# Optimization experiments

Measured on AMD Instinct MI355X. Metric: run time of the kernel, lower is better.

Reference implementation:

```python
import jax, jax.numpy as jnp
import numpy as np

CD_W1 = 1.0
CD_W2 = 1.0


def setup_inputs() -> dict:
    key = jax.random.key(0)
    k1, k2 = jax.random.split(key)
    B, N, M, D = 16, 4096, 4096, 3
    points1 = jax.random.normal(k1, (B, N, D), dtype=jnp.float32)
    points2 = jax.random.normal(k2, (B, M, D), dtype=jnp.float32)
    return {"points1": points1, "points2": points2}


def reference(points1, points2):
    # squared pairwise distances via |a|^2 + |b|^2 - 2 a.b (GEMM form)
    a2 = jnp.sum(points1 * points1, axis=-1)          # [B, N]
    b2 = jnp.sum(points2 * points2, axis=-1)          # [B, M]
    ab = jnp.einsum("bnd,bmd->bnm", points1, points2)  # [B, N, M]
    dist = a2[:, :, None] + b2[:, None, :] - 2.0 * ab   # [B, N, M]
    dist_min1 = jnp.min(dist, axis=2)                  # nearest in points2 for each point1
    dist_min2 = jnp.min(dist, axis=1)                  # nearest in points1 for each point2
    B = points1.shape[0]
    return (CD_W1 * jnp.sum(dist_min1) + CD_W2 * jnp.sum(dist_min2)) / B
```

## Files before the change

kernel.cpp:

```cpp
#include <hip/hip_runtime.h>

#define BQ     16
#define NPTS   4096
#define TOTAL  (BQ * NPTS)
#define NPART  128
#define SIDE_TILES    (TOTAL / 16)
#define PANEL_U4_SIDE ((size_t)SIDE_TILES * 32)
#define WS_MIN_BYTES  ((size_t)2 * TOTAL * 4)
#define WS_NEED (WS_MIN_BYTES + 2 * PANEL_U4_SIDE * 16 + (size_t)NPART * 4)

typedef __attribute__((ext_vector_type(8))) short short8;
typedef __attribute__((ext_vector_type(4))) float f32x4;

__device__ __forceinline__ unsigned short f2bf(float x) {
    union { float f; unsigned u; } v; v.f = x;
    unsigned r = v.u + 0x7FFFu + ((v.u >> 16) & 1u);
    return (unsigned short)(r >> 16);
}
__device__ __forceinline__ float bf2f(unsigned short h) {
    union { float f; unsigned u; } v; v.u = ((unsigned)h) << 16; return v.f;
}
#define BF_ONE 0x3F80

__device__ __forceinline__ uint4 make_bslots16(const float* __restrict__ pts,
                                               int tile, int lane32) {
    const int g = lane32 >> 4;
    const float* pp = pts + (size_t)(tile * 16 + (lane32 & 15)) * 3;
    const float x = pp[0], y = pp[1], z = pp[2];
    const unsigned short xh = f2bf(x), yh = f2bf(y), zh = f2bf(z);
    const unsigned short xl = f2bf(x - bf2f(xh)), yl = f2bf(y - bf2f(yh)),
                         zl = f2bf(z - bf2f(zh));
    const unsigned short m2xh = f2bf(-2.0f * bf2f(xh)), m2yh = f2bf(-2.0f * bf2f(yh)),
                         m2zh = f2bf(-2.0f * bf2f(zh));
    const unsigned short m2xl = f2bf(-2.0f * bf2f(xl)), m2yl = f2bf(-2.0f * bf2f(yl)),
                         m2zl = f2bf(-2.0f * bf2f(zl));
    const float s2 = fmaf(x, x, fmaf(y, y, z * z));
    const unsigned short s2h = f2bf(s2);
    const unsigned short s2l = f2bf(s2 - bf2f(s2h));
    unsigned short s[8];
    if (g == 0) { s[0]=m2xh; s[1]=m2yh; s[2]=m2zh; s[3]=m2xl;   s[4]=m2yl;   s[5]=m2zl; s[6]=m2xh; s[7]=m2yh; }
    else        { s[0]=m2zh; s[1]=BF_ONE; s[2]=BF_ONE; s[3]=s2h; s[4]=s2l;   s[5]=0;    s[6]=0;    s[7]=0;    }
    uint4 o;
    o.x = (unsigned)s[0] | ((unsigned)s[1] << 16);
    o.y = (unsigned)s[2] | ((unsigned)s[3] << 16);
    o.z = (unsigned)s[4] | ((unsigned)s[5] << 16);
    o.w = (unsigned)s[6] | ((unsigned)s[7] << 16);
    return o;
}

__device__ __forceinline__ short8 make_aslots16(const float* __restrict__ pts,
                                                int point, int g) {
    const float* pp = pts + (size_t)point * 3;
    const float x = pp[0], y = pp[1], z = pp[2];
    const unsigned short xh = f2bf(x), yh = f2bf(y), zh = f2bf(z);
    const unsigned short xl = f2bf(x - bf2f(xh)), yl = f2bf(y - bf2f(yh)),
                         zl = f2bf(z - bf2f(zh));
    const float s2 = fmaf(x, x, fmaf(y, y, z * z));
    const unsigned short s2h = f2bf(s2);
    const unsigned short s2l = f2bf(s2 - bf2f(s2h));
    unsigned short s[8];
    if (g == 0) { s[0]=xh; s[1]=yh; s[2]=zh; s[3]=xh;     s[4]=yh;     s[5]=zh; s[6]=xl; s[7]=yl; }
    else        { s[0]=zl; s[1]=s2h; s[2]=s2l; s[3]=BF_ONE; s[4]=BF_ONE; s[5]=0; s[6]=0; s[7]=0; }
    union { unsigned u[4]; short8 v; } o;
    o.u[0] = (unsigned)s[0] | ((unsigned)s[1] << 16);
    o.u[1] = (unsigned)s[2] | ((unsigned)s[3] << 16);
    o.u[2] = (unsigned)s[4] | ((unsigned)s[5] << 16);
    o.u[3] = (unsigned)s[6] | ((unsigned)s[7] << 16);
    return o.v;
}

__global__ __launch_bounds__(256) void cd_prep(const float* __restrict__ p1,
                                               const float* __restrict__ p2,
                                               unsigned* __restrict__ wsmin,
                                               uint4* __restrict__ panels) {
    const int tid = blockIdx.x * 256 + threadIdx.x;
    if (tid < 2 * TOTAL) wsmin[tid] = 0x7F800000u;
    const int side = tid >> 17;
    const int l    = tid & 131071;
    const float* pts = side ? p2 : p1;
    panels[tid] = make_bslots16(pts, l >> 5, l & 31);
}

__global__ __launch_bounds__(256, 4) void cd_pass(
        const float* __restrict__ p1, const float* __restrict__ p2,
        const uint4* __restrict__ panels, unsigned* __restrict__ wsmin) {
    const int dir  = blockIdx.y;
    const float* __restrict__ A = dir ? p2 : p1;
    const uint4* __restrict__ panel = panels + (dir ? 0 : PANEL_U4_SIDE);
    unsigned* __restrict__ outmin = wsmin + dir * TOTAL;

    const int bx   = blockIdx.x;
    const int b    = bx >> 5;
    const int rg   = (bx >> 2) & 7;
    const int cg   = bx & 3;
    const int wave = threadIdx.x >> 6;
    const int lane = threadIdx.x & 63;
    const int half = lane >> 5;

    const int rowbase = b * NPTS + rg * 512 + wave * 128;

    short8 az; { union { unsigned u[4]; short8 v; } z = {{0,0,0,0}}; az = z.v; }
    short8 a0=az,a1=az,a2=az,a3=az,a4=az,a5=az,a6=az,a7=az;
    if (half == 0) {
        const int g = (lane >> 4) & 1, r = lane & 15;
        a0 = make_aslots16(A, rowbase +   0 + r, g);
        a1 = make_aslots16(A, rowbase +  16 + r, g);
        a2 = make_aslots16(A, rowbase +  32 + r, g);
        a3 = make_aslots16(A, rowbase +  48 + r, g);
        a4 = make_aslots16(A, rowbase +  64 + r, g);
        a5 = make_aslots16(A, rowbase +  80 + r, g);
        a6 = make_aslots16(A, rowbase +  96 + r, g);
        a7 = make_aslots16(A, rowbase + 112 + r, g);
    }

    f32x4 zero = {0.0f, 0.0f, 0.0f, 0.0f};
    f32x4 r0,r1,r2,r3,r4,r5,r6,r7;
#pragma unroll
    for (int e = 0; e < 4; ++e) {
        r0[e]=3.0e38f; r1[e]=3.0e38f; r2[e]=3.0e38f; r3[e]=3.0e38f;
        r4[e]=3.0e38f; r5[e]=3.0e38f; r6[e]=3.0e38f; r7[e]=3.0e38f;
    }

    const uint4* __restrict__ bp =
        panel + (size_t)(b * 256 + cg * 64) * 32 + (lane & 31);

#define CD_COMPUTE(C0, C1)                                                   \
    do {                                                                     \
        const short8 bf0 = *reinterpret_cast<const short8*>(&(C0));          \
        const short8 bf1 = *reinterpret_cast<const short8*>(&(C1));          \
        f32x4 d0, d1;                                                        \
        d0 = __builtin_amdgcn_mfma_f32_16x16x32_bf16(a0, bf0, zero, 0,0,0);  \
        d1 = __builtin_amdgcn_mfma_f32_16x16x32_bf16(a0, bf1, zero, 0,0,0);  \
        _Pragma("unroll") for (int e = 0; e < 4; ++e)                        \
            r0[e] = fminf(r0[e], fminf(d0[e], d1[e]));                       \
        d0 = __builtin_amdgcn_mfma_f32_16x16x32_bf16(a1, bf0, zero, 0,0,0);  \
        d1 = __builtin_amdgcn_mfma_f32_16x16x32_bf16(a1, bf1, zero, 0,0,0);  \
        _Pragma("unroll") for (int e = 0; e < 4; ++e)                        \
            r1[e] = fminf(r1[e], fminf(d0[e], d1[e]));                       \
        d0 = __builtin_amdgcn_mfma_f32_16x16x32_bf16(a2, bf0, zero, 0,0,0);  \
        d1 = __builtin_amdgcn_mfma_f32_16x16x32_bf16(a2, bf1, zero, 0,0,0);  \
        _Pragma("unroll") for (int e = 0; e < 4; ++e)                        \
            r2[e] = fminf(r2[e], fminf(d0[e], d1[e]));                       \
        d0 = __builtin_amdgcn_mfma_f32_16x16x32_bf16(a3, bf0, zero, 0,0,0);  \
        d1 = __builtin_amdgcn_mfma_f32_16x16x32_bf16(a3, bf1, zero, 0,0,0);  \
        _Pragma("unroll") for (int e = 0; e < 4; ++e)                        \
            r3[e] = fminf(r3[e], fminf(d0[e], d1[e]));                       \
        d0 = __builtin_amdgcn_mfma_f32_16x16x32_bf16(a4, bf0, zero, 0,0,0);  \
        d1 = __builtin_amdgcn_mfma_f32_16x16x32_bf16(a4, bf1, zero, 0,0,0);  \
        _Pragma("unroll") for (int e = 0; e < 4; ++e)                        \
            r4[e] = fminf(r4[e], fminf(d0[e], d1[e]));                       \
        d0 = __builtin_amdgcn_mfma_f32_16x16x32_bf16(a5, bf0, zero, 0,0,0);  \
        d1 = __builtin_amdgcn_mfma_f32_16x16x32_bf16(a5, bf1, zero, 0,0,0);  \
        _Pragma("unroll") for (int e = 0; e < 4; ++e)                        \
            r5[e] = fminf(r5[e], fminf(d0[e], d1[e]));                       \
        d0 = __builtin_amdgcn_mfma_f32_16x16x32_bf16(a6, bf0, zero, 0,0,0);  \
        d1 = __builtin_amdgcn_mfma_f32_16x16x32_bf16(a6, bf1, zero, 0,0,0);  \
        _Pragma("unroll") for (int e = 0; e < 4; ++e)                        \
            r6[e] = fminf(r6[e], fminf(d0[e], d1[e]));                       \
        d0 = __builtin_amdgcn_mfma_f32_16x16x32_bf16(a7, bf0, zero, 0,0,0);  \
        d1 = __builtin_amdgcn_mfma_f32_16x16x32_bf16(a7, bf1, zero, 0,0,0);  \
        _Pragma("unroll") for (int e = 0; e < 4; ++e)                        \
            r7[e] = fminf(r7[e], fminf(d0[e], d1[e]));                       \
    } while (0)

    uint4 c0 = bp[0], c1 = bp[32];
    size_t off = 64;
#pragma unroll 1
    for (int i = 0; i < 31; ++i) {
        uint4 n0 = bp[off], n1 = bp[off + 32];
        off += 64;
        CD_COMPUTE(c0, c1);
        c0 = n0; c1 = n1;
    }
    CD_COMPUTE(c0, c1);
#undef CD_COMPUTE

    const int rgrp = lane >> 4;
#pragma unroll
    for (int s = 0; s < 8; ++s) {
        f32x4 rv = (s==0)?r0:(s==1)?r1:(s==2)?r2:(s==3)?r3:(s==4)?r4:(s==5)?r5:(s==6)?r6:r7;
#pragma unroll
        for (int e = 0; e < 4; ++e) {
            float v = rv[e];
            v = fminf(v, __shfl_xor(v, 1));
            v = fminf(v, __shfl_xor(v, 2));
            v = fminf(v, __shfl_xor(v, 4));
            v = fminf(v, __shfl_xor(v, 8));
            if ((lane & 15) == 0)
                atomicMin(&outmin[rowbase + s * 16 + rgrp * 4 + e],
                          __float_as_uint(fmaxf(v, 0.0f)));
        }
    }
}

__global__ __launch_bounds__(256) void cd_reduce1(const float* __restrict__ wsmin,
                                                  float* __restrict__ partial) {
    __shared__ float sred[256];
    const float4* __restrict__ v = (const float4*)wsmin;
    const int i = blockIdx.x * 256 + threadIdx.x;
    float4 x = v[i];
    sred[threadIdx.x] = (x.x + x.y) + (x.z + x.w);
    __syncthreads();
    for (int st = 128; st > 0; st >>= 1) {
        if (threadIdx.x < st) sred[threadIdx.x] += sred[threadIdx.x + st];
        __syncthreads();
    }
    if (threadIdx.x == 0) partial[blockIdx.x] = sred[0];
}

__global__ __launch_bounds__(NPART) void cd_reduce2(const float* __restrict__ partial,
                                                    float* __restrict__ out) {
    __shared__ float sred[NPART];
    sred[threadIdx.x] = partial[threadIdx.x];
    __syncthreads();
    for (int st = NPART / 2; st > 0; st >>= 1) {
        if (threadIdx.x < st) sred[threadIdx.x] += sred[threadIdx.x + st];
        __syncthreads();
    }
    if (threadIdx.x == 0) out[0] = sred[0] * (1.0f / (float)BQ);
}

__global__ __launch_bounds__(256) void cd_init_ws(unsigned int* __restrict__ ws) {
    ws[blockIdx.x * 256 + threadIdx.x] = 0x7F800000u;
}
#define F_APT 8
__global__ __launch_bounds__(256) void cd_min_lds(
        const float* __restrict__ p1, const float* __restrict__ p2,
        unsigned int* __restrict__ wsmin) {
    const int dir = blockIdx.y;
    const float* __restrict__ Aset = dir ? p2 : p1;
    const float* __restrict__ Bset = dir ? p1 : p2;
    unsigned int* __restrict__ outmin = wsmin + dir * TOTAL;
    const int atile = blockIdx.x / 16;
    const int mtile = blockIdx.x % 16;
    const int a0 = atile * 2048;
    const int m0 = (a0 / NPTS) * NPTS + mtile * 256;
    __shared__ float4 sbf[256];
    {
        const float* bpn = Bset + (size_t)(m0 + threadIdx.x) * 3;
        float bx = bpn[0], by = bpn[1], bz = bpn[2];
        sbf[threadIdx.x] = make_float4(-2.0f*bx, -2.0f*by, -2.0f*bz,
                                       fmaf(bx,bx,fmaf(by,by,bz*bz)));
    }
    __syncthreads();
    float ax[F_APT], ay[F_APT], az_[F_APT], q2[F_APT], mn[F_APT];
#pragma unroll
    for (int k = 0; k < F_APT; ++k) {
        const int ai = a0 + k*256 + threadIdx.x;
        const float* ap = Aset + (size_t)ai * 3;
        ax[k]=ap[0]; ay[k]=ap[1]; az_[k]=ap[2];
        q2[k]=fmaf(ax[k],ax[k],fmaf(ay[k],ay[k],az_[k]*az_[k]));
        mn[k]=3.0e38f;
    }
#pragma unroll 2
    for (int j = 0; j < 256; j += 2) {
        const float4 b0 = sbf[j], b1 = sbf[j+1];
#pragma unroll
        for (int k = 0; k < F_APT; ++k) {
            float d0 = fmaf(az_[k],b0.z,b0.w); d0=fmaf(ay[k],b0.y,d0); d0=fmaf(ax[k],b0.x,d0);
            float d1 = fmaf(az_[k],b1.z,b1.w); d1=fmaf(ay[k],b1.y,d1); d1=fmaf(ax[k],b1.x,d1);
            mn[k] = fminf(fminf(mn[k], d0), d1);
        }
    }
#pragma unroll
    for (int k = 0; k < F_APT; ++k) {
        const int ai = a0 + k*256 + threadIdx.x;
        atomicMin(&outmin[ai], __float_as_uint(fmaxf(q2[k]+mn[k], 0.0f)));
    }
}
__global__ __launch_bounds__(1024) void cd_reduce_single(const float* __restrict__ wsmin,
                                                         float* __restrict__ out) {
    __shared__ float sred[1024];
    const float4* __restrict__ v = (const float4*)wsmin;
    float s = 0.0f;
    for (int i = threadIdx.x; i < (2*TOTAL)/4; i += 1024) {
        float4 x = v[i]; s += (x.x + x.y) + (x.z + x.w);
    }
    sred[threadIdx.x] = s;
    __syncthreads();
    for (int st = 512; st > 0; st >>= 1) {
        if (threadIdx.x < st) sred[threadIdx.x] += sred[threadIdx.x + st];
        __syncthreads();
    }
    if (threadIdx.x == 0) out[0] = sred[0] * (1.0f / (float)BQ);
}

extern "C" void kernel_launch(void* const* d_in, const int* in_sizes, int n_in,
                              void* d_out, int out_size, void* d_ws, size_t ws_size,
                              hipStream_t stream) {
    const float* p1 = (const float*)d_in[0];
    const float* p2 = (const float*)d_in[1];
    float* out = (float*)d_out;

    if (ws_size >= WS_NEED) {
        unsigned* wsmin = (unsigned*)d_ws;
        uint4* panels  = (uint4*)((char*)d_ws + WS_MIN_BYTES);
        float* partial = (float*)((char*)d_ws + WS_MIN_BYTES + 2 * PANEL_U4_SIDE * 16);

        cd_prep<<<1024, 256, 0, stream>>>(p1, p2, wsmin, panels);
        dim3 grid(512, 2, 1);
        cd_pass<<<grid, 256, 0, stream>>>(p1, p2, panels, wsmin);
        cd_reduce1<<<128, 256, 0, stream>>>((const float*)wsmin, partial);
        cd_reduce2<<<1, NPART, 0, stream>>>(partial, out);
    } else {
        unsigned* wsmin = (unsigned*)d_ws;
        cd_init_ws<<<(2 * TOTAL) / 256, 256, 0, stream>>>(wsmin);
        dim3 grid(512, 2, 1);
        cd_min_lds<<<grid, 256, 0, stream>>>(p1, p2, wsmin);
        cd_reduce_single<<<1, 1024, 0, stream>>>((const float*)wsmin, out);
    }
}
```

Before: 43.39 us.

## Fuse panel prep into main kernel via LDS and replace atomics with partial-min buffers

After: 41.96 us. -3.3%, faster.

```diff
diff --git a/kernel.cpp b/kernel.cpp
--- a/kernel.cpp
+++ b/kernel.cpp
@@ -4,10 +4,9 @@
 #define NPTS   4096
 #define TOTAL  (BQ * NPTS)
 #define NPART  128
-#define SIDE_TILES    (TOTAL / 16)
-#define PANEL_U4_SIDE ((size_t)SIDE_TILES * 32)
-#define WS_MIN_BYTES  ((size_t)2 * TOTAL * 4)
-#define WS_NEED (WS_MIN_BYTES + 2 * PANEL_U4_SIDE * 16 + (size_t)NPART * 4)
+
+#define ROWMIN_FLOATS ((size_t)8 * TOTAL)
+#define WS_NEED (ROWMIN_FLOATS * 4 + (size_t)NPART * 4)
 
 typedef __attribute__((ext_vector_type(8))) short short8;
 typedef __attribute__((ext_vector_type(4))) float f32x4;
@@ -69,25 +68,12 @@
     return o.v;
 }
 
-__global__ __launch_bounds__(256) void cd_prep(const float* __restrict__ p1,
-                                               const float* __restrict__ p2,
-                                               unsigned* __restrict__ wsmin,
-                                               uint4* __restrict__ panels) {
-    const int tid = blockIdx.x * 256 + threadIdx.x;
-    if (tid < 2 * TOTAL) wsmin[tid] = 0x7F800000u;
-    const int side = tid >> 17;
-    const int l    = tid & 131071;
-    const float* pts = side ? p2 : p1;
-    panels[tid] = make_bslots16(pts, l >> 5, l & 31);
-}
-
-__global__ __launch_bounds__(256, 4) void cd_pass(
+__global__ __launch_bounds__(256, 4) void cd_main(
         const float* __restrict__ p1, const float* __restrict__ p2,
-        const uint4* __restrict__ panels, unsigned* __restrict__ wsmin) {
+        float* __restrict__ rowmin) {
     const int dir  = blockIdx.y;
-    const float* __restrict__ A = dir ? p2 : p1;
-    const uint4* __restrict__ panel = panels + (dir ? 0 : PANEL_U4_SIDE);
-    unsigned* __restrict__ outmin = wsmin + dir * TOTAL;
+    const float* __restrict__ A  = dir ? p2 : p1;
+    const float* __restrict__ Bp = dir ? p1 : p2;
 
     const int bx   = blockIdx.x;
     const int b    = bx >> 5;
@@ -96,6 +82,15 @@
     const int wave = threadIdx.x >> 6;
     const int lane = threadIdx.x & 63;
     const int half = lane >> 5;
+
+    __shared__ uint4 spanel[64 * 32];
+
+    const float* __restrict__ Bbase = Bp + (size_t)(b * NPTS + cg * 1024) * 3;
+#pragma unroll
+    for (int k = 0; k < 8; ++k) {
+        const int s = threadIdx.x + k * 256;
+        spanel[s] = make_bslots16(Bbase, s >> 5, s & 31);
+    }
 
     const int rowbase = b * NPTS + rg * 512 + wave * 128;
 
@@ -121,8 +116,7 @@
         r4[e]=3.0e38f; r5[e]=3.0e38f; r6[e]=3.0e38f; r7[e]=3.0e38f;
     }
 
-    const uint4* __restrict__ bp =
-        panel + (size_t)(b * 256 + cg * 64) * 32 + (lane & 31);
+    __syncthreads();
 
 #define CD_COMPUTE(C0, C1)                                                   \
     do {                                                                     \
@@ -163,18 +157,21 @@
             r7[e] = fminf(r7[e], fminf(d0[e], d1[e]));                       \
     } while (0)
 
-    uint4 c0 = bp[0], c1 = bp[32];
-    size_t off = 64;
+    const int sl = lane & 31;
+    int idx = wave * 16;
+    uint4 c0 = spanel[idx * 32 + sl], c1 = spanel[(idx + 1) * 32 + sl];
 #pragma unroll 1
     for (int i = 0; i < 31; ++i) {
-        uint4 n0 = bp[off], n1 = bp[off + 32];
-        off += 64;
+        const int nidx = (idx + 2) & 63;
+        uint4 n0 = spanel[nidx * 32 + sl];
+        uint4 n1 = spanel[(nidx + 1) * 32 + sl];
         CD_COMPUTE(c0, c1);
-        c0 = n0; c1 = n1;
+        c0 = n0; c1 = n1; idx = nidx;
     }
     CD_COMPUTE(c0, c1);
 #undef CD_COMPUTE
 
+    float* __restrict__ outr = rowmin + (size_t)(dir * 4 + cg) * TOTAL;
     const int rgrp = lane >> 4;
 #pragma unroll
     for (int s = 0; s < 8; ++s) {
@@ -187,19 +184,26 @@
             v = fminf(v, __shfl_xor(v, 4));
             v = fminf(v, __shfl_xor(v, 8));
             if ((lane & 15) == 0)
-                atomicMin(&outmin[rowbase + s * 16 + rgrp * 4 + e],
-                          __float_as_uint(fmaxf(v, 0.0f)));
+                outr[rowbase + s * 16 + rgrp * 4 + e] = fmaxf(v, 0.0f);
         }
     }
 }
 
-__global__ __launch_bounds__(256) void cd_reduce1(const float* __restrict__ wsmin,
+__global__ __launch_bounds__(256) void cd_combine(const float* __restrict__ rowmin,
                                                   float* __restrict__ partial) {
     __shared__ float sred[256];
-    const float4* __restrict__ v = (const float4*)wsmin;
-    const int i = blockIdx.x * 256 + threadIdx.x;
-    float4 x = v[i];
-    sred[threadIdx.x] = (x.x + x.y) + (x.z + x.w);
+    const int tid = blockIdx.x * 256 + threadIdx.x;
+    float s = 0.0f;
+#pragma unroll
+    for (int k = 0; k < 4; ++k) {
+        const int i   = tid + k * 32768;
+        const int d   = i >> 16;
+        const int row = i & (TOTAL - 1);
+        const float* base = rowmin + (size_t)d * 4 * TOTAL + row;
+        s += fminf(fminf(base[0], base[TOTAL]),
+                   fminf(base[2 * TOTAL], base[3 * TOTAL]));
+    }
+    sred[threadIdx.x] = s;
     __syncthreads();
     for (int st = 128; st > 0; st >>= 1) {
         if (threadIdx.x < st) sred[threadIdx.x] += sred[threadIdx.x + st];
@@ -208,8 +212,8 @@
     if (threadIdx.x == 0) partial[blockIdx.x] = sred[0];
 }
 
-__global__ __launch_bounds__(NPART) void cd_reduce2(const float* __restrict__ partial,
-                                                    float* __restrict__ out) {
+__global__ __launch_bounds__(NPART) void cd_final(const float* __restrict__ partial,
+                                                  float* __restrict__ out) {
     __shared__ float sred[NPART];
     sred[threadIdx.x] = partial[threadIdx.x];
     __syncthreads();
@@ -293,15 +297,13 @@
     float* out = (float*)d_out;
 
     if (ws_size >= WS_NEED) {
-        unsigned* wsmin = (unsigned*)d_ws;
-        uint4* panels  = (uint4*)((char*)d_ws + WS_MIN_BYTES);
-        float* partial = (float*)((char*)d_ws + WS_MIN_BYTES + 2 * PANEL_U4_SIDE * 16);
-
-        cd_prep<<<1024, 256, 0, stream>>>(p1, p2, wsmin, panels);
+        float* rowmin  = (float*)d_ws;
+        float* partial = (float*)((char*)d_ws + ROWMIN_FLOATS * 4);
+
         dim3 grid(512, 2, 1);
-        cd_pass<<<grid, 256, 0, stream>>>(p1, p2, panels, wsmin);
-        cd_reduce1<<<128, 256, 0, stream>>>((const float*)wsmin, partial);
-        cd_reduce2<<<1, NPART, 0, stream>>>(partial, out);
+        cd_main<<<grid, 256, 0, stream>>>(p1, p2, rowmin);
+        cd_combine<<<128, 256, 0, stream>>>(rowmin, partial);
+        cd_final<<<1, NPART, 0, stream>>>(partial, out);
     } else {
         unsigned* wsmin = (unsigned*)d_ws;
         cd_init_ws<<<(2 * TOTAL) / 256, 256, 0, stream>>>(wsmin);
```
